# Kernel tuning notes

Hardware: AMD Instinct MI355X
Metric: run time of the kernel (lower is better)

The kernel has to match this reference:

```python
import jax, jax.numpy as jnp
import numpy as np

B, N, FEAT, HID = 1024, 128, 512, 256


def setup_inputs() -> dict:
    key = jax.random.key(0)
    k1, k2, k3, k4, k5, k6 = jax.random.split(key, 6)
    x = jax.random.normal(k1, (B, FEAT), dtype=jnp.float32)
    labels = jax.random.randint(k2, (B,), 0, N, dtype=jnp.int64)
    W_proj = jax.random.normal(k3, (FEAT, HID), dtype=jnp.float32) / np.sqrt(FEAT)
    b_proj = jax.random.normal(k4, (HID,), dtype=jnp.float32) * 0.01
    means = jax.random.normal(k5, (N, HID), dtype=jnp.float32)
    # inverse covariances must be SPD so sqrt(dist_sq) is real
    A = jax.random.normal(k6, (N, HID, HID), dtype=jnp.float32)
    inv_covs = jnp.einsum('nij,nkj->nik', A, A) / HID + 0.1 * jnp.eye(HID, dtype=jnp.float32)
    return {"x": x, "labels": labels, "W_proj": W_proj, "b_proj": b_proj,
            "means": means, "inv_covs": inv_covs}


def reference(x, labels, W_proj, b_proj, means, inv_covs):
    b = x.shape[0]
    n = means.shape[0]
    x_proj = x @ W_proj + b_proj                       # (b, hid)
    delta = x_proj[:, None, :] - means[None, :, :]     # (b, n, hid)
    # batched Mahalanobis quadratic form
    dist_sq = jnp.einsum('bni,nij,bnj->bn', delta, inv_covs, delta)
    distmat = jnp.sqrt(dist_sq + 1e-12)                # (b, n)
    center_mask = (labels[:, None] == jnp.arange(n)[None, :]).astype(distmat.dtype)
    loss = jnp.clip(distmat * center_mask, 1e-12, 1e12).sum() / b
    return loss, distmat
```

## Files before the change

### kernel.cpp

```cpp
#include <hip/hip_runtime.h>
#include <hip/hip_bf16.h>

#define B_    1024
#define N_    128
#define FEAT_ 512
#define HID_  256

typedef __bf16 bf16x8 __attribute__((ext_vector_type(8)));
typedef float  f32x4  __attribute__((ext_vector_type(4)));

__device__ __forceinline__ unsigned int f2bf(float f) {
    unsigned int u = __float_as_uint(f);
    u += 0x7fffu + ((u >> 16) & 1u);
    return u >> 16;
}
__device__ __forceinline__ unsigned int pack2(float a, float b) {
    return f2bf(a) | (f2bf(b) << 16);
}

__global__ __launch_bounds__(512, 4) void prep_kernel(
    const float* __restrict__ x, const float* __restrict__ W,
    const float* __restrict__ bias, const float* __restrict__ means,
    const float* __restrict__ invcov,
    float* __restrict__ xp, unsigned short* __restrict__ xbf,
    unsigned short* __restrict__ Mbf, float* __restrict__ v2,
    float* __restrict__ cpart, float* __restrict__ out)
{
    const int t = threadIdx.x;
    if (blockIdx.x < 512) {
        __shared__ float xs[2][FEAT_];
        const int b0 = blockIdx.x * 2;
        if (t < 256)
            ((float4*)&xs[0][0])[t] = ((const float4*)(x + (size_t)b0 * FEAT_))[t];
        if (blockIdx.x == 0 && t == 0) out[0] = (float)(N_ - 1) * 1e-12f;
        __syncthreads();
        const int row = t >> 8;
        const int h   = t & 255;
        const float* __restrict__ xr = &xs[row][0];
        float acc = bias[h];
        float Ab[16], Bb[16];
        auto LD = [&](float (&buf)[16], int g) {
            #pragma unroll
            for (int u = 0; u < 16; ++u) buf[u] = W[(size_t)(g * 16 + u) * HID_ + h];
        };
        auto FM = [&](const float (&buf)[16], int g) {
            #pragma unroll
            for (int u = 0; u < 16; ++u) acc += xr[g * 16 + u] * buf[u];
        };
        LD(Ab, 0);
        for (int g = 0; g < 30; g += 2) {
            LD(Bb, g + 1);
            FM(Ab, g);
            LD(Ab, g + 2);
            FM(Bb, g + 1);
        }
        LD(Bb, 31);
        FM(Ab, 30);
        FM(Bb, 31);
        const int gr = b0 + row;
        xp [(size_t)gr * HID_ + h] = acc;
        xbf[(size_t)gr * HID_ + h] = (unsigned short)f2bf(acc);
    } else {
        __shared__ float sv[32][33];
        __shared__ float sw[4];
        const int cb  = blockIdx.x - 512;
        const int n   = cb >> 3;
        const int jg2 = cb & 7;
        const float* Mn = invcov + (size_t)n * (HID_ * HID_) + (size_t)jg2 * 32 * HID_;
        const float* mu = means + (size_t)n * HID_;
        unsigned short* Mb = Mbf + (size_t)n * (HID_ * HID_) + (size_t)jg2 * 32 * HID_;
        const int gc = t & 31;
        const int r0 = t >> 5;
        const float4 mk0 = *(const float4*)(mu + gc * 8);
        const float4 mk1 = *(const float4*)(mu + gc * 8 + 4);
        #pragma unroll
        for (int i = 0; i < 2; ++i) {
            const int row = r0 + i * 16;
            const float* src = Mn + (size_t)row * HID_ + gc * 8;
            const float4 a = *(const float4*)src;
            const float4 b = *(const float4*)(src + 4);
            const int g2 = gc ^ ((row & 7) << 2);
            *(uint4*)(Mb + (size_t)row * HID_ + g2 * 8) =
                make_uint4(pack2(a.x, a.y), pack2(a.z, a.w), pack2(b.x, b.y), pack2(b.z, b.w));
            sv[row][gc] = a.x * mk0.x + a.y * mk0.y + a.z * mk0.z + a.w * mk0.w
                        + b.x * mk1.x + b.y * mk1.y + b.z * mk1.z + b.w * mk1.w;
        }
        __syncthreads();
        if (t < 256) {
            const int row = t >> 3;
            const int i0  = (t & 7) * 4;
            float v = sv[row][i0] + sv[row][i0 + 1] + sv[row][i0 + 2] + sv[row][i0 + 3];
            v += __shfl_xor(v, 1);
            v += __shfl_xor(v, 2);
            v += __shfl_xor(v, 4);
            const int j = jg2 * 32 + row;
            if ((t & 7) == 0) v2[(size_t)n * HID_ + j] = 2.f * v;
            float cc = ((t & 7) == 0) ? v * mu[j] : 0.f;
            cc += __shfl_xor(cc, 8);
            cc += __shfl_xor(cc, 16);
            cc += __shfl_xor(cc, 32);
            if ((t & 63) == 0) sw[t >> 6] = cc;
        }
        __syncthreads();
        if (t == 0) cpart[cb] = sw[0] + sw[1] + sw[2] + sw[3];
    }
}

__global__ __launch_bounds__(512, 4) void dist_kernel(
    const float* __restrict__ xp, const unsigned short* __restrict__ xbf,
    const unsigned short* __restrict__ Mbf, const float* __restrict__ v2,
    float* __restrict__ p)
{
    extern __shared__ unsigned short Ms[];

    const int tid  = threadIdx.x;
    const int bh   = blockIdx.x;
    const int jh   = blockIdx.y;
    const int n    = blockIdx.z;
    const int wave = tid >> 6;
    const int lane = tid & 63;
    const int q    = lane >> 4;
    const int l    = lane & 15;

    const unsigned short* src = Mbf + (size_t)n * (HID_ * HID_) + (size_t)jh * 32768;
    #pragma unroll
    for (int i = 0; i < 8; ++i) {
        const int c = i * 8 + wave;
        __builtin_amdgcn_global_load_lds(
            (const __attribute__((address_space(1))) unsigned int*)(src + (size_t)c * 512 + lane * 8),
            (__attribute__((address_space(3))) unsigned int*)&Ms[c * 512],
            16, 0, 0);
    }

    bf16x8 afrag[2][8];
    #pragma unroll
    for (int rb = 0; rb < 2; ++rb) {
        const unsigned short* xr = xbf + (size_t)(bh * 256 + wave * 32 + rb * 16 + l) * HID_;
        #pragma unroll
        for (int kk = 0; kk < 8; ++kk)
            afrag[rb][kk] = *(const bf16x8*)(xr + kk * 32 + q * 8);
    }
    float v2l[8];
    #pragma unroll
    for (int ct = 0; ct < 8; ++ct)
        v2l[ct] = v2[(size_t)n * HID_ + jh * 128 + ct * 16 + l];

    __syncthreads();

    float part[8];
    #pragma unroll
    for (int i = 0; i < 8; ++i) part[i] = 0.f;

    const size_t xbase = (size_t)(bh * 256 + wave * 32 + q * 4) * HID_ + jh * 128 + l;

    #pragma unroll
    for (int ct = 0; ct < 8; ++ct) {
        float xl[8];
        #pragma unroll
        for (int rb = 0; rb < 2; ++rb)
            #pragma unroll
            for (int r = 0; r < 4; ++r)
                xl[rb * 4 + r] = xp[xbase + (size_t)(rb * 16 + r) * HID_ + ct * 16];

        f32x4 acc0 = {0.f,0.f,0.f,0.f}, acc1 = {0.f,0.f,0.f,0.f};
        #pragma unroll
        for (int kk = 0; kk < 8; ++kk) {
            const bf16x8 bfrag = *(const bf16x8*)&Ms[(ct * 16 + l) * HID_ +
                                                     (((kk * 4 + q) ^ ((l & 7) << 2)) << 3)];
            acc0 = __builtin_amdgcn_mfma_f32_16x16x32_bf16(afrag[0][kk], bfrag, acc0, 0, 0, 0);
            acc1 = __builtin_amdgcn_mfma_f32_16x16x32_bf16(afrag[1][kk], bfrag, acc1, 0, 0, 0);
        }
        const float vv = v2l[ct];
        #pragma unroll
        for (int r = 0; r < 4; ++r) {
            part[r]     += (acc0[r] - vv) * xl[r];
            part[4 + r] += (acc1[r] - vv) * xl[4 + r];
        }
    }

    #pragma unroll
    for (int i = 0; i < 8; ++i) {
        float v = part[i];
        v += __shfl_xor(v, 1);
        v += __shfl_xor(v, 2);
        v += __shfl_xor(v, 4);
        v += __shfl_xor(v, 8);
        part[i] = v;
    }
    if (l == 0) {
        float* pb = p + (size_t)jh * (B_ * N_);
        #pragma unroll
        for (int i = 0; i < 8; ++i) {
            const int row = bh * 256 + wave * 32 + (i >> 2) * 16 + q * 4 + (i & 3);
            pb[(size_t)row * N_ + n] = part[i];
        }
    }
}

__global__ __launch_bounds__(256) void finalize_kernel(
    const float* __restrict__ p, const float* __restrict__ cpart,
    const int* __restrict__ labels, float* __restrict__ out)
{
    __shared__ float sc[128];
    __shared__ float ls[4];
    const int t = threadIdx.x;
    if (t < 128) {
        float s = 0.f;
        #pragma unroll
        for (int g = 0; g < 8; ++g) s += cpart[t * 8 + g];
        sc[t] = s;
    }
    __syncthreads();
    const int i = blockIdx.x * 256 + t;
    const int n = i & (N_ - 1);
    const int b = i >> 7;
    const float d = sqrtf(p[i] + p[B_ * N_ + i] + sc[n] + 1e-12f);
    out[1 + i] = d;
    float sel = (labels[b] == n) ? d : 0.f;
    #pragma unroll
    for (int m = 1; m <= 32; m <<= 1) sel += __shfl_xor(sel, m);
    if ((t & 63) == 0) ls[t >> 6] = sel;
    __syncthreads();
    if (t == 0) atomicAdd(out, (ls[0] + ls[1] + ls[2] + ls[3]) * (1.f / (float)B_));
}

extern "C" void kernel_launch(void* const* d_in, const int* in_sizes, int n_in,
                              void* d_out, int out_size, void* d_ws, size_t ws_size,
                              hipStream_t stream) {
    const float* x      = (const float*)d_in[0];
    const int*   labels = (const int*)d_in[1];
    const float* W      = (const float*)d_in[2];
    const float* bias   = (const float*)d_in[3];
    const float* means  = (const float*)d_in[4];
    const float* invcov = (const float*)d_in[5];
    float* out = (float*)d_out;

    char* ws = (char*)d_ws;
    unsigned short* Mbf   = (unsigned short*)(ws);
    float*          xp    = (float*)         (ws + 16777216);
    unsigned short* xbf   = (unsigned short*)(ws + 17825792);
    float*          v2    = (float*)         (ws + 18350080);
    float*          cpart = (float*)         (ws + 18481152);
    float*          p     = (float*)         (ws + 18489344);

    constexpr int DIST_LDS = 128 * HID_ * 2;
    (void)hipFuncSetAttribute((const void*)dist_kernel,
                              hipFuncAttributeMaxDynamicSharedMemorySize, DIST_LDS);

    prep_kernel<<<dim3(1536), 512, 0, stream>>>(x, W, bias, means, invcov,
                                                xp, xbf, Mbf, v2, cpart, out);
    dist_kernel<<<dim3(4, 2, N_), 512, DIST_LDS, stream>>>(xp, xbf, Mbf, v2, p);
    finalize_kernel<<<dim3((B_ * N_) / 256), 256, 0, stream>>>(p, cpart, labels, out);
}
```

Before: 144.0 us.

## Fuse finalize into dist kernel with double-buffered LDS and reshape prep

Removes the separate finalize kernel by computing sqrt, output write and loss accumulation in the dist kernel epilogue. Dist no longer splits the hidden dimension across blocks; instead it streams the inverse covariance through a two-slot LDS buffer in four phases, overlapping loads with MFMA work. Prep is rebalanced to 256-thread blocks with float2 vectorized projection and finer covariance conversion blocks. The trade-off is fewer dist blocks, more syncs, and per-element atomics for the loss.

After: 210.9 us. +46.5%, slower.

```diff
diff --git a/kernel.cpp b/kernel.cpp
--- a/kernel.cpp
+++ b/kernel.cpp
@@ -18,7 +18,7 @@
     return f2bf(a) | (f2bf(b) << 16);
 }
 
-__global__ __launch_bounds__(512, 4) void prep_kernel(
+__global__ __launch_bounds__(256, 6) void prep_kernel(
     const float* __restrict__ x, const float* __restrict__ W,
     const float* __restrict__ bias, const float* __restrict__ means,
     const float* __restrict__ invcov,
@@ -27,55 +27,23 @@
     float* __restrict__ cpart, float* __restrict__ out)
 {
     const int t = threadIdx.x;
-    if (blockIdx.x < 512) {
-        __shared__ float xs[2][FEAT_];
-        const int b0 = blockIdx.x * 2;
-        if (t < 256)
-            ((float4*)&xs[0][0])[t] = ((const float4*)(x + (size_t)b0 * FEAT_))[t];
-        if (blockIdx.x == 0 && t == 0) out[0] = (float)(N_ - 1) * 1e-12f;
-        __syncthreads();
-        const int row = t >> 8;
-        const int h   = t & 255;
-        const float* __restrict__ xr = &xs[row][0];
-        float acc = bias[h];
-        float Ab[16], Bb[16];
-        auto LD = [&](float (&buf)[16], int g) {
-            #pragma unroll
-            for (int u = 0; u < 16; ++u) buf[u] = W[(size_t)(g * 16 + u) * HID_ + h];
-        };
-        auto FM = [&](const float (&buf)[16], int g) {
-            #pragma unroll
-            for (int u = 0; u < 16; ++u) acc += xr[g * 16 + u] * buf[u];
-        };
-        LD(Ab, 0);
-        for (int g = 0; g < 30; g += 2) {
-            LD(Bb, g + 1);
-            FM(Ab, g);
-            LD(Ab, g + 2);
-            FM(Bb, g + 1);
-        }
-        LD(Bb, 31);
-        FM(Ab, 30);
-        FM(Bb, 31);
-        const int gr = b0 + row;
-        xp [(size_t)gr * HID_ + h] = acc;
-        xbf[(size_t)gr * HID_ + h] = (unsigned short)f2bf(acc);
-    } else {
-        __shared__ float sv[32][33];
-        __shared__ float sw[4];
-        const int cb  = blockIdx.x - 512;
-        const int n   = cb >> 3;
-        const int jg2 = cb & 7;
-        const float* Mn = invcov + (size_t)n * (HID_ * HID_) + (size_t)jg2 * 32 * HID_;
+    if (blockIdx.x < 2048) {
+        __shared__ float sv[16][33];
+        __shared__ float sw[2];
+        const int cb = blockIdx.x;
+        const int n  = cb >> 4;
+        const int jg = cb & 15;
+        const float* Mn = invcov + (size_t)n * (HID_ * HID_) + (size_t)jg * 16 * HID_;
         const float* mu = means + (size_t)n * HID_;
-        unsigned short* Mb = Mbf + (size_t)n * (HID_ * HID_) + (size_t)jg2 * 32 * HID_;
+        unsigned short* Mb = Mbf + (size_t)n * (HID_ * HID_) + (size_t)jg * 16 * HID_;
         const int gc = t & 31;
         const int r0 = t >> 5;
         const float4 mk0 = *(const float4*)(mu + gc * 8);
         const float4 mk1 = *(const float4*)(mu + gc * 8 + 4);
+        if (cb == 0 && t == 0) out[0] = (float)(N_ - 1) * 1e-12f;
         #pragma unroll
         for (int i = 0; i < 2; ++i) {
-            const int row = r0 + i * 16;
+            const int row = r0 + i * 8;
             const float* src = Mn + (size_t)row * HID_ + gc * 8;
             const float4 a = *(const float4*)src;
             const float4 b = *(const float4*)(src + 4);
@@ -86,14 +54,14 @@
                         + b.x * mk1.x + b.y * mk1.y + b.z * mk1.z + b.w * mk1.w;
         }
         __syncthreads();
-        if (t < 256) {
+        if (t < 128) {
             const int row = t >> 3;
             const int i0  = (t & 7) * 4;
             float v = sv[row][i0] + sv[row][i0 + 1] + sv[row][i0 + 2] + sv[row][i0 + 3];
             v += __shfl_xor(v, 1);
             v += __shfl_xor(v, 2);
             v += __shfl_xor(v, 4);
-            const int j = jg2 * 32 + row;
+            const int j = jg * 16 + row;
             if ((t & 7) == 0) v2[(size_t)n * HID_ + j] = 2.f * v;
             float cc = ((t & 7) == 0) ? v * mu[j] : 0.f;
             cc += __shfl_xor(cc, 8);
@@ -102,35 +70,79 @@
             if ((t & 63) == 0) sw[t >> 6] = cc;
         }
         __syncthreads();
-        if (t == 0) cpart[cb] = sw[0] + sw[1] + sw[2] + sw[3];
+        if (t == 0) cpart[cb] = sw[0] + sw[1];
+    } else {
+        __shared__ float xs[2][FEAT_];
+        const int pb = blockIdx.x - 2048;
+        const int b0 = pb * 2;
+        ((float4*)&xs[0][0])[t] = ((const float4*)(x + (size_t)b0 * FEAT_))[t];
+        __syncthreads();
+        const int row = t >> 7;
+        const int h2  = t & 127;
+        const float* __restrict__ xr = &xs[row][0];
+        const float2* Wv = (const float2*)W;
+        float2 acc = ((const float2*)bias)[h2];
+        float2 Ab[8], Bb[8];
+        auto LD = [&](float2 (&buf)[8], int g) {
+            #pragma unroll
+            for (int u = 0; u < 8; ++u) buf[u] = Wv[(size_t)(g * 8 + u) * 128 + h2];
+        };
+        auto FM = [&](const float2 (&buf)[8], int g) {
+            #pragma unroll
+            for (int u = 0; u < 8; ++u) {
+                const float xv = xr[g * 8 + u];
+                acc.x += xv * buf[u].x;
+                acc.y += xv * buf[u].y;
+            }
+        };
+        LD(Ab, 0);
+        for (int g = 0; g < 62; g += 2) {
+            LD(Bb, g + 1);
+            FM(Ab, g);
+            LD(Ab, g + 2);
+            FM(Bb, g + 1);
+        }
+        LD(Bb, 63);
+        FM(Ab, 62);
+        FM(Bb, 63);
+        const int gr = b0 + row;
+        ((float2*)(xp + (size_t)gr * HID_))[h2] = acc;
+        *(unsigned int*)(xbf + (size_t)gr * HID_ + h2 * 2) = pack2(acc.x, acc.y);
     }
 }
 
 __global__ __launch_bounds__(512, 4) void dist_kernel(
     const float* __restrict__ xp, const unsigned short* __restrict__ xbf,
     const unsigned short* __restrict__ Mbf, const float* __restrict__ v2,
-    float* __restrict__ p)
+    const float* __restrict__ cpart, const int* __restrict__ labels,
+    float* __restrict__ out)
 {
     extern __shared__ unsigned short Ms[];
+    __shared__ float cn;
 
     const int tid  = threadIdx.x;
     const int bh   = blockIdx.x;
-    const int jh   = blockIdx.y;
-    const int n    = blockIdx.z;
+    const int n    = blockIdx.y;
     const int wave = tid >> 6;
     const int lane = tid & 63;
     const int q    = lane >> 4;
     const int l    = lane & 15;
 
-    const unsigned short* src = Mbf + (size_t)n * (HID_ * HID_) + (size_t)jh * 32768;
-    #pragma unroll
-    for (int i = 0; i < 8; ++i) {
+    const unsigned short* src = Mbf + (size_t)n * (HID_ * HID_);
+    #pragma unroll
+    for (int i = 0; i < 4; ++i) {
         const int c = i * 8 + wave;
         __builtin_amdgcn_global_load_lds(
             (const __attribute__((address_space(1))) unsigned int*)(src + (size_t)c * 512 + lane * 8),
             (__attribute__((address_space(3))) unsigned int*)&Ms[c * 512],
             16, 0, 0);
     }
+    if (tid == 0) {
+        float s = 0.f;
+        #pragma unroll
+        for (int g = 0; g < 16; ++g) s += cpart[n * 16 + g];
+        cn = s;
+    }
 
     bf16x8 afrag[2][8];
     #pragma unroll
@@ -140,10 +152,6 @@
         for (int kk = 0; kk < 8; ++kk)
             afrag[rb][kk] = *(const bf16x8*)(xr + kk * 32 + q * 8);
     }
-    float v2l[8];
-    #pragma unroll
-    for (int ct = 0; ct < 8; ++ct)
-        v2l[ct] = v2[(size_t)n * HID_ + jh * 128 + ct * 16 + l];
 
     __syncthreads();
 
@@ -151,31 +159,52 @@
     #pragma unroll
     for (int i = 0; i < 8; ++i) part[i] = 0.f;
 
-    const size_t xbase = (size_t)(bh * 256 + wave * 32 + q * 4) * HID_ + jh * 128 + l;
-
-    #pragma unroll
-    for (int ct = 0; ct < 8; ++ct) {
-        float xl[8];
-        #pragma unroll
-        for (int rb = 0; rb < 2; ++rb)
-            #pragma unroll
-            for (int r = 0; r < 4; ++r)
-                xl[rb * 4 + r] = xp[xbase + (size_t)(rb * 16 + r) * HID_ + ct * 16];
-
-        f32x4 acc0 = {0.f,0.f,0.f,0.f}, acc1 = {0.f,0.f,0.f,0.f};
-        #pragma unroll
-        for (int kk = 0; kk < 8; ++kk) {
-            const bf16x8 bfrag = *(const bf16x8*)&Ms[(ct * 16 + l) * HID_ +
-                                                     (((kk * 4 + q) ^ ((l & 7) << 2)) << 3)];
-            acc0 = __builtin_amdgcn_mfma_f32_16x16x32_bf16(afrag[0][kk], bfrag, acc0, 0, 0, 0);
-            acc1 = __builtin_amdgcn_mfma_f32_16x16x32_bf16(afrag[1][kk], bfrag, acc1, 0, 0, 0);
-        }
-        const float vv = v2l[ct];
-        #pragma unroll
-        for (int r = 0; r < 4; ++r) {
-            part[r]     += (acc0[r] - vv) * xl[r];
-            part[4 + r] += (acc1[r] - vv) * xl[4 + r];
-        }
+    const size_t xbase = (size_t)(bh * 256 + wave * 32 + q * 4) * HID_ + l;
+
+    #pragma unroll
+    for (int p = 0; p < 4; ++p) {
+        if (p < 3) {
+            const unsigned short* sp = src + (size_t)(p + 1) * 16384;
+            #pragma unroll
+            for (int i = 0; i < 4; ++i) {
+                const int c = i * 8 + wave;
+                __builtin_amdgcn_global_load_lds(
+                    (const __attribute__((address_space(1))) unsigned int*)(sp + (size_t)c * 512 + lane * 8),
+                    (__attribute__((address_space(3))) unsigned int*)&Ms[((p + 1) & 1) * 16384 + c * 512],
+                    16, 0, 0);
+            }
+        }
+        float v2p[4];
+        #pragma unroll
+        for (int ctl = 0; ctl < 4; ++ctl)
+            v2p[ctl] = v2[(size_t)n * HID_ + (p * 4 + ctl) * 16 + l];
+
+        #pragma unroll
+        for (int ctl = 0; ctl < 4; ++ctl) {
+            const int ct = p * 4 + ctl;
+            float xl[8];
+            #pragma unroll
+            for (int rb = 0; rb < 2; ++rb)
+                #pragma unroll
+                for (int r = 0; r < 4; ++r)
+                    xl[rb * 4 + r] = xp[xbase + (size_t)(rb * 16 + r) * HID_ + ct * 16];
+
+            f32x4 acc0 = {0.f,0.f,0.f,0.f}, acc1 = {0.f,0.f,0.f,0.f};
+            #pragma unroll
+            for (int kk = 0; kk < 8; ++kk) {
+                const bf16x8 bfrag = *(const bf16x8*)&Ms[(p & 1) * 16384 + (ctl * 16 + l) * HID_ +
+                                                         (((kk * 4 + q) ^ ((l & 7) << 2)) << 3)];
+                acc0 = __builtin_amdgcn_mfma_f32_16x16x32_bf16(afrag[0][kk], bfrag, acc0, 0, 0, 0);
+                acc1 = __builtin_amdgcn_mfma_f32_16x16x32_bf16(afrag[1][kk], bfrag, acc1, 0, 0, 0);
+            }
+            const float vv = v2p[ctl];
+            #pragma unroll
+            for (int r = 0; r < 4; ++r) {
+                part[r]     += (acc0[r] - vv) * xl[r];
+                part[4 + r] += (acc1[r] - vv) * xl[4 + r];
+            }
+        }
+        if (p < 3) __syncthreads();
     }
 
     #pragma unroll
@@ -188,40 +217,15 @@
         part[i] = v;
     }
     if (l == 0) {
-        float* pb = p + (size_t)jh * (B_ * N_);
+        const float cc = cn;
         #pragma unroll
         for (int i = 0; i < 8; ++i) {
             const int row = bh * 256 + wave * 32 + (i >> 2) * 16 + q * 4 + (i & 3);
-            pb[(size_t)row * N_ + n] = part[i];
-        }
-    }
-}
-
-__global__ __launch_bounds__(256) void finalize_kernel(
-    const float* __restrict__ p, const float* __restrict__ cpart,
-    const int* __restrict__ labels, float* __restrict__ out)
-{
-    __shared__ float sc[128];
-    __shared__ float ls[4];
-    const int t = threadIdx.x;
-    if (t < 128) {
-        float s = 0.f;
-        #pragma unroll
-        for (int g = 0; g < 8; ++g) s += cpart[t * 8 + g];
-        sc[t] = s;
-    }
-    __syncthreads();
-    const int i = blockIdx.x * 256 + t;
-    const int n = i & (N_ - 1);
-    const int b = i >> 7;
-    const float d = sqrtf(p[i] + p[B_ * N_ + i] + sc[n] + 1e-12f);
-    out[1 + i] = d;
-    float sel = (labels[b] == n) ? d : 0.f;
-    #pragma unroll
-    for (int m = 1; m <= 32; m <<= 1) sel += __shfl_xor(sel, m);
-    if ((t & 63) == 0) ls[t >> 6] = sel;
-    __syncthreads();
-    if (t == 0) atomicAdd(out, (ls[0] + ls[1] + ls[2] + ls[3]) * (1.f / (float)B_));
+            const float d = sqrtf(part[i] + cc + 1e-12f);
+            out[1 + (size_t)row * N_ + n] = d;
+            if (labels[row] == n) atomicAdd(out, d * (1.f / (float)B_));
+        }
+    }
 }
 
 extern "C" void kernel_launch(void* const* d_in, const int* in_sizes, int n_in,
@@ -241,14 +245,13 @@
     unsigned short* xbf   = (unsigned short*)(ws + 17825792);
     float*          v2    = (float*)         (ws + 18350080);
     float*          cpart = (float*)         (ws + 18481152);
-    float*          p     = (float*)         (ws + 18489344);
-
-    constexpr int DIST_LDS = 128 * HID_ * 2;
+
+    constexpr int DIST_LDS = 2 * 16384 * 2;
     (void)hipFuncSetAttribute((const void*)dist_kernel,
                               hipFuncAttributeMaxDynamicSharedMemorySize, DIST_LDS);
 
-    prep_kernel<<<dim3(1536), 512, 0, stream>>>(x, W, bias, means, invcov,
+    prep_kernel<<<dim3(2560), 256, 0, stream>>>(x, W, bias, means, invcov,
                                                 xp, xbf, Mbf, v2, cpart, out);
-    dist_kernel<<<dim3(4, 2, N_), 512, DIST_LDS, stream>>>(xp, xbf, Mbf, v2, p);
-    finalize_kernel<<<dim3((B_ * N_) / 256), 256, 0, stream>>>(p, cpart, labels, out);
-}
+    dist_kernel<<<dim3(4, N_), 512, DIST_LDS, stream>>>(xp, xbf, Mbf, v2,
+                                                        cpart, labels, out);
+}
```

## Retile projection GEMM so each block computes 16 rows over half the hidden dim

Applied to the files above, without the earlier changes.

The projection part of prep_kernel moves from 512 blocks of 2 rows each to 128 blocks, each covering 16 batch rows and 128 hidden columns. Each thread now computes a 2x2 output tile using float2 weight loads, so every W element fetched is reused across two rows and each block reuses W across 16 rows. This cuts redundant W traffic. The shared buffer grows to 32 KB and is unified with the covariance branch, which may lower occupancy for those blocks. There are also far fewer projection blocks, so that phase has less parallelism.

Result: slower. 154.4 us (+7.2%).

```diff
diff --git a/kernel.cpp b/kernel.cpp
--- a/kernel.cpp
+++ b/kernel.cpp
@@ -26,44 +26,61 @@
     unsigned short* __restrict__ Mbf, float* __restrict__ v2,
     float* __restrict__ cpart, float* __restrict__ out)
 {
+    __shared__ float smem[16 * FEAT_];
     const int t = threadIdx.x;
-    if (blockIdx.x < 512) {
-        __shared__ float xs[2][FEAT_];
-        const int b0 = blockIdx.x * 2;
-        if (t < 256)
-            ((float4*)&xs[0][0])[t] = ((const float4*)(x + (size_t)b0 * FEAT_))[t];
-        if (blockIdx.x == 0 && t == 0) out[0] = (float)(N_ - 1) * 1e-12f;
+    if (blockIdx.x < 128) {
+        float (*xs)[FEAT_] = (float (*)[FEAT_])smem;
+        const int pb    = blockIdx.x;
+        const int b0    = (pb >> 1) * 16;
+        const int hbase = (pb & 1) * 128;
+        {
+            const float4* xsrc = (const float4*)(x + (size_t)b0 * FEAT_);
+            #pragma unroll
+            for (int i = 0; i < 4; ++i)
+                ((float4*)smem)[t + i * 512] = xsrc[t + i * 512];
+        }
+        if (pb == 0 && t == 0) out[0] = (float)(N_ - 1) * 1e-12f;
         __syncthreads();
-        const int row = t >> 8;
-        const int h   = t & 255;
-        const float* __restrict__ xr = &xs[row][0];
-        float acc = bias[h];
-        float Ab[16], Bb[16];
-        auto LD = [&](float (&buf)[16], int g) {
-            #pragma unroll
-            for (int u = 0; u < 16; ++u) buf[u] = W[(size_t)(g * 16 + u) * HID_ + h];
+        const int w = t >> 6;
+        const int l = t & 63;
+        const float* __restrict__ xr0 = &xs[w * 2][0];
+        const float* __restrict__ xr1 = &xs[w * 2 + 1][0];
+        const float2* Wp = (const float2*)(W + hbase);
+        float2 a0 = ((const float2*)(bias + hbase))[l];
+        float2 a1 = a0;
+        float2 Ab[8], Bb[8];
+        auto LD = [&](float2 (&buf)[8], int g) {
+            #pragma unroll
+            for (int u = 0; u < 8; ++u) buf[u] = Wp[(size_t)(g * 8 + u) * 128 + l];
         };
-        auto FM = [&](const float (&buf)[16], int g) {
-            #pragma unroll
-            for (int u = 0; u < 16; ++u) acc += xr[g * 16 + u] * buf[u];
+        auto FM = [&](const float2 (&buf)[8], int g) {
+            #pragma unroll
+            for (int u = 0; u < 8; ++u) {
+                const float x0 = xr0[g * 8 + u];
+                const float x1 = xr1[g * 8 + u];
+                a0.x += x0 * buf[u].x;  a0.y += x0 * buf[u].y;
+                a1.x += x1 * buf[u].x;  a1.y += x1 * buf[u].y;
+            }
         };
         LD(Ab, 0);
-        for (int g = 0; g < 30; g += 2) {
+        for (int g = 0; g < 62; g += 2) {
             LD(Bb, g + 1);
             FM(Ab, g);
             LD(Ab, g + 2);
             FM(Bb, g + 1);
         }
-        LD(Bb, 31);
-        FM(Ab, 30);
-        FM(Bb, 31);
-        const int gr = b0 + row;
-        xp [(size_t)gr * HID_ + h] = acc;
-        xbf[(size_t)gr * HID_ + h] = (unsigned short)f2bf(acc);
+        LD(Bb, 63);
+        FM(Ab, 62);
+        FM(Bb, 63);
+        const int r0g = b0 + w * 2;
+        ((float2*)(xp + (size_t)r0g * HID_ + hbase))[l]       = a0;
+        ((float2*)(xp + (size_t)(r0g + 1) * HID_ + hbase))[l] = a1;
+        *(unsigned int*)(xbf + (size_t)r0g * HID_ + hbase + l * 2)       = pack2(a0.x, a0.y);
+        *(unsigned int*)(xbf + (size_t)(r0g + 1) * HID_ + hbase + l * 2) = pack2(a1.x, a1.y);
     } else {
-        __shared__ float sv[32][33];
-        __shared__ float sw[4];
-        const int cb  = blockIdx.x - 512;
+        float (*sv)[33] = (float (*)[33])smem;
+        float* sw = smem + 32 * 33;
+        const int cb  = blockIdx.x - 128;
         const int n   = cb >> 3;
         const int jg2 = cb & 7;
         const float* Mn = invcov + (size_t)n * (HID_ * HID_) + (size_t)jg2 * 32 * HID_;
@@ -247,7 +264,7 @@
     (void)hipFuncSetAttribute((const void*)dist_kernel,
                               hipFuncAttributeMaxDynamicSharedMemorySize, DIST_LDS);
 
-    prep_kernel<<<dim3(1536), 512, 0, stream>>>(x, W, bias, means, invcov,
+    prep_kernel<<<dim3(1152), 512, 0, stream>>>(x, W, bias, means, invcov,
                                                 xp, xbf, Mbf, v2, cpart, out);
     dist_kernel<<<dim3(4, 2, N_), 512, DIST_LDS, stream>>>(xp, xbf, Mbf, v2, p);
     finalize_kernel<<<dim3((B_ * N_) / 256), 256, 0, stream>>>(p, cpart, labels, out);
```

## Compute input projection with split-bf16 MFMA instead of scalar FP32 FMA

Applied to the files above, without the earlier changes.

A new pre-kernel transposes W, splits it into bf16 high and low parts, and stores them in a swizzled layout. The projection part of prep_kernel now loads those tiles into LDS with global_load_lds and computes x@W with three bf16 MFMAs per k-step (hi*hi, hi*lo, lo*hi), which approximates fp32 accuracy. Projection blocks drop from 512 to 128 and the scalar FMA loop over W is gone. The cost is an extra kernel launch, a lower-precision projection, and a reused workspace offset: Wt_hi starts at the same address as p, so correctness depends on dist_kernel writing p only after prep has finished reading it.

After: 136.8 us. 1.05x faster.

```diff
diff --git a/kernel.cpp b/kernel.cpp
--- a/kernel.cpp
+++ b/kernel.cpp
@@ -18,52 +18,110 @@
     return f2bf(a) | (f2bf(b) << 16);
 }
 
+union U4V8 { uint4 u; bf16x8 v; };
+
+__global__ __launch_bounds__(256) void wprep_kernel(
+    const float* __restrict__ W, unsigned short* __restrict__ Wt_hi,
+    unsigned short* __restrict__ Wt_lo, float* __restrict__ out)
+{
+    const int t = threadIdx.x;
+    const int g = blockIdx.x;
+    if (g == 0 && t == 0) out[0] = (float)(N_ - 1) * 1e-12f;
+    float v[8];
+    #pragma unroll
+    for (int j = 0; j < 8; ++j) v[j] = W[(size_t)(g * 8 + j) * HID_ + t];
+    unsigned int hu[4], lu[4];
+    #pragma unroll
+    for (int i = 0; i < 4; ++i) {
+        const unsigned int u0 = __float_as_uint(v[2 * i]);
+        const unsigned int u1 = __float_as_uint(v[2 * i + 1]);
+        hu[i] = (u0 >> 16) | (u1 & 0xFFFF0000u);
+        const float l0 = v[2 * i]     - __uint_as_float(u0 & 0xFFFF0000u);
+        const float l1 = v[2 * i + 1] - __uint_as_float(u1 & 0xFFFF0000u);
+        lu[i] = pack2(l0, l1);
+    }
+    const int g2 = g ^ ((t & 7) << 2);
+    const size_t off = (size_t)t * FEAT_ + g2 * 8;
+    *(uint4*)(Wt_hi + off) = make_uint4(hu[0], hu[1], hu[2], hu[3]);
+    *(uint4*)(Wt_lo + off) = make_uint4(lu[0], lu[1], lu[2], lu[3]);
+}
+
 __global__ __launch_bounds__(512, 4) void prep_kernel(
-    const float* __restrict__ x, const float* __restrict__ W,
-    const float* __restrict__ bias, const float* __restrict__ means,
-    const float* __restrict__ invcov,
+    const float* __restrict__ x, const unsigned short* __restrict__ Wt_hi,
+    const unsigned short* __restrict__ Wt_lo, const float* __restrict__ bias,
+    const float* __restrict__ means, const float* __restrict__ invcov,
     float* __restrict__ xp, unsigned short* __restrict__ xbf,
     unsigned short* __restrict__ Mbf, float* __restrict__ v2,
-    float* __restrict__ cpart, float* __restrict__ out)
+    float* __restrict__ cpart)
 {
+    extern __shared__ char dyn[];
     const int t = threadIdx.x;
-    if (blockIdx.x < 512) {
-        __shared__ float xs[2][FEAT_];
-        const int b0 = blockIdx.x * 2;
-        if (t < 256)
-            ((float4*)&xs[0][0])[t] = ((const float4*)(x + (size_t)b0 * FEAT_))[t];
-        if (blockIdx.x == 0 && t == 0) out[0] = (float)(N_ - 1) * 1e-12f;
+    if (blockIdx.x < 128) {
+        unsigned short* Ms = (unsigned short*)dyn;
+        const int pb   = blockIdx.x;
+        const int bg   = pb >> 4;
+        const int ht   = pb & 15;
+        const int wave = t >> 6;
+        const int lane = t & 63;
+        const int q    = lane >> 4;
+        const int l    = lane & 15;
+
+        #pragma unroll
+        for (int i = 0; i < 4; ++i) {
+            const int cc   = i * 8 + wave;
+            const int term = cc >> 4, lc = cc & 15;
+            const unsigned short* s = (term ? Wt_lo : Wt_hi)
+                                      + (size_t)ht * (16 * FEAT_) + lc * 512 + lane * 8;
+            __builtin_amdgcn_global_load_lds(
+                (const __attribute__((address_space(1))) unsigned int*)s,
+                (__attribute__((address_space(3))) unsigned int*)&Ms[term * 8192 + lc * 512],
+                16, 0, 0);
+        }
+
+        const int row = bg * 128 + wave * 16 + l;
+        const float* __restrict__ xr = x + (size_t)row * FEAT_;
+        f32x4 acc = {0.f, 0.f, 0.f, 0.f};
         __syncthreads();
-        const int row = t >> 8;
-        const int h   = t & 255;
-        const float* __restrict__ xr = &xs[row][0];
-        float acc = bias[h];
-        float Ab[16], Bb[16];
-        auto LD = [&](float (&buf)[16], int g) {
+
+        #pragma unroll
+        for (int kk = 0; kk < 16; ++kk) {
+            const float4 xa = *(const float4*)(xr + kk * 32 + q * 8);
+            const float4 xb = *(const float4*)(xr + kk * 32 + q * 8 + 4);
+            const float vv[8] = {xa.x, xa.y, xa.z, xa.w, xb.x, xb.y, xb.z, xb.w};
+            U4V8 xh, xl;
+            unsigned int hu[4], lu[4];
             #pragma unroll
-            for (int u = 0; u < 16; ++u) buf[u] = W[(size_t)(g * 16 + u) * HID_ + h];
-        };
-        auto FM = [&](const float (&buf)[16], int g) {
-            #pragma unroll
-            for (int u = 0; u < 16; ++u) acc += xr[g * 16 + u] * buf[u];
-        };
-        LD(Ab, 0);
-        for (int g = 0; g < 30; g += 2) {
-            LD(Bb, g + 1);
-            FM(Ab, g);
-            LD(Ab, g + 2);
-            FM(Bb, g + 1);
-        }
-        LD(Bb, 31);
-        FM(Ab, 30);
-        FM(Bb, 31);
-        const int gr = b0 + row;
-        xp [(size_t)gr * HID_ + h] = acc;
-        xbf[(size_t)gr * HID_ + h] = (unsigned short)f2bf(acc);
+            for (int i = 0; i < 4; ++i) {
+                const unsigned int u0 = __float_as_uint(vv[2 * i]);
+                const unsigned int u1 = __float_as_uint(vv[2 * i + 1]);
+                hu[i] = (u0 >> 16) | (u1 & 0xFFFF0000u);
+                const float l0 = vv[2 * i]     - __uint_as_float(u0 & 0xFFFF0000u);
+                const float l1 = vv[2 * i + 1] - __uint_as_float(u1 & 0xFFFF0000u);
+                lu[i] = pack2(l0, l1);
+            }
+            xh.u = make_uint4(hu[0], hu[1], hu[2], hu[3]);
+            xl.u = make_uint4(lu[0], lu[1], lu[2], lu[3]);
+            const int g2 = (((kk * 4 + q) ^ ((l & 7) << 2)) << 3);
+            U4V8 bh, bl;
+            bh.u = *(const uint4*)&Ms[l * FEAT_ + g2];
+            bl.u = *(const uint4*)&Ms[8192 + l * FEAT_ + g2];
+            acc = __builtin_amdgcn_mfma_f32_16x16x32_bf16(xh.v, bh.v, acc, 0, 0, 0);
+            acc = __builtin_amdgcn_mfma_f32_16x16x32_bf16(xh.v, bl.v, acc, 0, 0, 0);
+            acc = __builtin_amdgcn_mfma_f32_16x16x32_bf16(xl.v, bh.v, acc, 0, 0, 0);
+        }
+        const int h  = ht * 16 + l;
+        const float bb = bias[h];
+        #pragma unroll
+        for (int r = 0; r < 4; ++r) {
+            const int ro = bg * 128 + wave * 16 + q * 4 + r;
+            const float val = acc[r] + bb;
+            xp [(size_t)ro * HID_ + h] = val;
+            xbf[(size_t)ro * HID_ + h] = (unsigned short)f2bf(val);
+        }
     } else {
-        __shared__ float sv[32][33];
-        __shared__ float sw[4];
-        const int cb  = blockIdx.x - 512;
+        float (*sv)[33] = (float (*)[33])dyn;
+        float* sw = (float*)(dyn + 32 * 33 * 4);
+        const int cb  = blockIdx.x - 128;
         const int n   = cb >> 3;
         const int jg2 = cb & 7;
         const float* Mn = invcov + (size_t)n * (HID_ * HID_) + (size_t)jg2 * 32 * HID_;
@@ -242,13 +300,16 @@
     float*          v2    = (float*)         (ws + 18350080);
     float*          cpart = (float*)         (ws + 18481152);
     float*          p     = (float*)         (ws + 18489344);
+    unsigned short* Wt_hi = (unsigned short*)(ws + 18489344);
+    unsigned short* Wt_lo = (unsigned short*)(ws + 18751488);
 
     constexpr int DIST_LDS = 128 * HID_ * 2;
     (void)hipFuncSetAttribute((const void*)dist_kernel,
                               hipFuncAttributeMaxDynamicSharedMemorySize, DIST_LDS);
 
-    prep_kernel<<<dim3(1536), 512, 0, stream>>>(x, W, bias, means, invcov,
-                                                xp, xbf, Mbf, v2, cpart, out);
+    wprep_kernel<<<dim3(64), 256, 0, stream>>>(W, Wt_hi, Wt_lo, out);
+    prep_kernel<<<dim3(1152), 512, 32768, stream>>>(x, Wt_hi, Wt_lo, bias, means, invcov,
+                                                    xp, xbf, Mbf, v2, cpart);
     dist_kernel<<<dim3(4, 2, N_), 512, DIST_LDS, stream>>>(xp, xbf, Mbf, v2, p);
     finalize_kernel<<<dim3((B_ * N_) / 256), 256, 0, stream>>>(p, cpart, labels, out);
 }
```
